# Kernel optimization log

Hardware: AMD Instinct MI355X
Metric: run time of the kernel (lower is better)

## Reference

```python
import jax, jax.numpy as jnp
import numpy as np

H = 8      # heads
D = 64     # dim_head
N0 = 1024  # modality-0 tokens
N1 = 1024  # modality-1 tokens
N = N0 + N1  # == token_num
DI = H * D   # dim_inner = 512


def setup_inputs() -> dict:
    key = jax.random.key(0)
    ks = jax.random.split(key, 10)
    s = 0.02
    return {
        "x0": jax.random.normal(ks[0], (1, N0, 512), jnp.float32),
        "x1": jax.random.normal(ks[1], (1, N1, 512), jnp.float32),
        "mask0": jnp.ones((1, N0), jnp.bool_),
        "mask1": jnp.ones((1, N1), jnp.bool_),
        "attn_dist": jax.random.normal(ks[2], (1, N, N), jnp.float32),
        "W_in0": jax.random.normal(ks[3], (512, 3 * DI), jnp.float32) * s,
        "W_in1": jax.random.normal(ks[4], (512, 3 * DI), jnp.float32) * s,
        "W_tau": jax.random.normal(ks[5], (DI, N * H), jnp.float32) * s,
        "b_tau": jax.random.normal(ks[6], (N * H,), jnp.float32) * s,
        "W_out0": jax.random.normal(ks[7], (DI, 512), jnp.float32) * s,
        "W_out1": jax.random.normal(ks[8], (DI, 512), jnp.float32) * s,
    }


def _split_heads(qkv, B, n):
    # (B, n, 3*H*D) -> (3, B, H, n, D)   [matches Rearrange 'b n (qkv h d) -> qkv b h n d']
    return qkv.reshape(B, n, 3, H, D).transpose(2, 0, 3, 1, 4)


def reference(x0, x1, mask0, mask1, attn_dist, W_in0, W_in1, W_tau, b_tau, W_out0, W_out1):
    B = x0.shape[0]
    qkv0 = _split_heads(x0 @ W_in0, B, N0)
    qkv1 = _split_heads(x1 @ W_in1, B, N1)
    qkv = jnp.concatenate([qkv0, qkv1], axis=3)  # pack along token axis -> (3,B,H,N,D)
    q, k, v = qkv[0], qkv[1], qkv[2]
    mask = jnp.concatenate([mask0, mask1], axis=1)  # (B, N)

    sim = jnp.einsum('bhid,bhjd->bhij', q, k) / jnp.sqrt(jnp.array(D, q.dtype))
    neg = -jnp.finfo(sim.dtype).max
    sim = jnp.where(mask[:, None, None, :], sim, neg)

    # taus: raw row-major reshape of q (B,H,N,D) -> (B,N,H*D), as in torch .reshape
    q_flat = q.reshape(B, N, H * D)
    taus = (q_flat @ W_tau + b_tau).reshape(B, N, N, H)
    bias = (taus * attn_dist[..., None]).transpose(0, 3, 1, 2)  # (B,H,N,N)
    sim = sim - bias

    attn = jax.nn.softmax(sim.astype(jnp.float32), axis=-1).astype(sim.dtype)
    out = jnp.einsum('bhij,bhjd->bhid', attn, v)
    out = out.transpose(0, 2, 1, 3).reshape(B, N, H * D)  # merge heads

    out0 = out[:, :N0] @ W_out0
    out1 = out[:, N0:] @ W_out1
    return (out0, out1)
```

## Files before the change

kernel.cpp:

```cpp
#include <hip/hip_runtime.h>
#include <stdint.h>

typedef __bf16 bf16;
typedef __bf16 bf16x8 __attribute__((ext_vector_type(8)));
typedef float f32x4 __attribute__((ext_vector_type(4)));
typedef unsigned short u16x8 __attribute__((ext_vector_type(8)));

#define MFMA16(a, b, c) __builtin_amdgcn_mfma_f32_16x16x32_bf16(a, b, c, 0, 0, 0)

#define WAIT_VM8 0x0F78
#define WAIT_VM0 0x0F70

static __device__ __forceinline__ bf16x8 lds_frag(const unsigned short* p) {
  return __builtin_bit_cast(bf16x8, *(const u16x8*)p);
}

static __device__ __forceinline__ bf16x8 gmem_frag(const bf16* p) {
  return __builtin_bit_cast(bf16x8, *(const u16x8*)p);
}

static __device__ __forceinline__ u16x8 cvt8(const float* p) {
  f32x4 a = *(const f32x4*)p;
  f32x4 b = *(const f32x4*)(p + 4);
  u16x8 r;
#pragma unroll
  for (int e = 0; e < 4; ++e) {
    r[e] = __builtin_bit_cast(unsigned short, (bf16)a[e]);
    r[4 + e] = __builtin_bit_cast(unsigned short, (bf16)b[e]);
  }
  return r;
}

__global__ __launch_bounds__(256) void prep_kernel(
    const float* __restrict__ Wti, const float* __restrict__ btau,
    const float* __restrict__ x0, const float* __restrict__ x1,
    const float* __restrict__ Win0, const float* __restrict__ Win1,
    const float* __restrict__ Wo0, const float* __restrict__ Wo1,
    bf16* __restrict__ Wto, float* __restrict__ bto, bf16* __restrict__ xb,
    bf16* __restrict__ Winb0, bf16* __restrict__ Winb1,
    bf16* __restrict__ Wob0, bf16* __restrict__ Wob1) {
  const int b = blockIdx.x;
  const int tid = threadIdx.x;
  __shared__ unsigned short shm[8 * 32 * 72];

  if (b < 512) {
    const int c0 = (b & 7) * 64;
    const int j0 = (b >> 3) * 32;
#pragma unroll
    for (int it = 0; it < 8; ++it) {
      int idx = it * 256 + tid;
      int c = idx >> 5, j = idx & 31;
      u16x8 v = cvt8(Wti + (size_t)(c0 + c) * 16384 + (j0 + j) * 8);
#pragma unroll
      for (int h = 0; h < 8; ++h) shm[(h * 32 + j) * 72 + c] = v[h];
    }
    __syncthreads();
#pragma unroll
    for (int it = 0; it < 8; ++it) {
      int chunk = it * 256 + tid;
      int row = chunk >> 3, ck = chunk & 7;
      int h = row >> 5, j = row & 31;
      u16x8 v = *(const u16x8*)&shm[row * 72 + ck * 8];
      *(u16x8*)((unsigned short*)Wto + (size_t)(h * 2048 + j0 + j) * 512 + c0 + ck * 8) = v;
    }
    if ((b & 7) == 0) {
      int j = tid >> 3, h = tid & 7;
      bto[h * 2048 + j0 + j] = btau[(j0 + j) * 8 + h];
    }
  } else if (b < 896) {
    int t = b - 512;
    const float* W = t < 192 ? Win0 : Win1;
    bf16* Wb = t < 192 ? Winb0 : Winb1;
    t = t < 192 ? t : t - 192;
    const int c0 = (t & 7) * 64, n0 = (t >> 3) * 64;
#pragma unroll
    for (int it = 0; it < 2; ++it) {
      int idx = it * 256 + tid;
      int c = idx >> 3, nn = idx & 7;
      u16x8 v = cvt8(W + (size_t)(c0 + c) * 1536 + n0 + nn * 8);
#pragma unroll
      for (int e = 0; e < 8; ++e) shm[(nn * 8 + e) * 72 + c] = v[e];
    }
    __syncthreads();
#pragma unroll
    for (int it = 0; it < 2; ++it) {
      int idx = it * 256 + tid;
      int n = idx >> 3, ck = idx & 7;
      *(u16x8*)((unsigned short*)Wb + (size_t)(n0 + n) * 512 + c0 + ck * 8) =
          *(const u16x8*)&shm[n * 72 + ck * 8];
    }
  } else if (b < 1408) {
    int t = b - 896;
    const float* src = t < 256 ? x0 : x1;
    size_t dst0 = t < 256 ? 0 : 524288;
    int tt = t < 256 ? t : t - 256;
    size_t off = (size_t)tt * 2048 + tid * 8;
    u16x8 v = cvt8(src + off);
    *(u16x8*)((unsigned short*)xb + dst0 + off) = v;
  } else {
    int t = b - 1408;
    const float* W = t < 64 ? Wo0 : Wo1;
    bf16* Wb = t < 64 ? Wob0 : Wob1;
    t &= 63;
    const int c0 = (t & 7) * 64, n0 = (t >> 3) * 64;
#pragma unroll
    for (int it = 0; it < 2; ++it) {
      int idx = it * 256 + tid;
      int c = idx >> 3, nn = idx & 7;
      u16x8 v = cvt8(W + (size_t)(c0 + c) * 512 + n0 + nn * 8);
#pragma unroll
      for (int e = 0; e < 8; ++e) shm[(nn * 8 + e) * 72 + c] = v[e];
    }
    __syncthreads();
#pragma unroll
    for (int it = 0; it < 2; ++it) {
      int idx = it * 256 + tid;
      int n = idx >> 3, ck = idx & 7;
      *(u16x8*)((unsigned short*)Wb + (size_t)(n0 + n) * 512 + c0 + ck * 8) =
          *(const u16x8*)&shm[n * 72 + ck * 8];
    }
  }
}

__global__ __launch_bounds__(256) void qkv_gemm(
    const bf16* __restrict__ xb, const bf16* __restrict__ Winb0, const bf16* __restrict__ Winb1,
    bf16* __restrict__ Qb, bf16* __restrict__ Kb, bf16* __restrict__ Vt_g) {
  const int i0 = blockIdx.x * 128, c0 = blockIdx.y * 128;
  const bf16* Bm = (i0 < 1024) ? Winb0 : Winb1;
  const int tid = threadIdx.x;
  const int lane = tid & 63, wave = tid >> 6;
  const int l16 = lane & 15, quad = lane >> 4;
  const int mrow = (wave & 1) * 64, ncol = (wave >> 1) * 64;
  __shared__ unsigned short As[2][128 * 64];
  __shared__ unsigned short Bs[2][128 * 64];
  f32x4 acc[4][4] = {};

#define QKV_STAGE(bb, kt)                                                               \
  do {                                                                                  \
    const int k0s = (kt) * 64;                                                          \
    _Pragma("unroll") for (int c = 0; c < 4; ++c) {                                     \
      int s = c * 256 + tid;                                                            \
      int row = s >> 3, pos = s & 7;                                                    \
      int kc = pos ^ (row & 7);                                                         \
      __builtin_amdgcn_global_load_lds(                                                 \
          (const unsigned int*)(xb + (size_t)(i0 + row) * 512 + k0s + kc * 8),          \
          (unsigned int*)&As[bb][s * 8], 16, 0, 0);                                     \
      __builtin_amdgcn_global_load_lds(                                                 \
          (const unsigned int*)(Bm + (size_t)(c0 + row) * 512 + k0s + kc * 8),          \
          (unsigned int*)&Bs[bb][s * 8], 16, 0, 0);                                     \
    }                                                                                   \
  } while (0)

  QKV_STAGE(0, 0);
  for (int t = 0; t < 8; ++t) {
    const int cur = t & 1;
    if (t < 7) {
      QKV_STAGE(cur ^ 1, t + 1);
      __builtin_amdgcn_s_waitcnt(WAIT_VM8);
    } else {
      __builtin_amdgcn_s_waitcnt(WAIT_VM0);
    }
    __builtin_amdgcn_s_barrier();
#pragma unroll
    for (int kb = 0; kb < 2; ++kb) {
      bf16x8 a[4], b[4];
#pragma unroll
      for (int mt = 0; mt < 4; ++mt) {
        int row = mrow + mt * 16 + l16;
        a[mt] = lds_frag(&As[cur][row * 64 + (((kb * 4 + quad) ^ (row & 7)) * 8)]);
      }
#pragma unroll
      for (int nt = 0; nt < 4; ++nt) {
        int row = ncol + nt * 16 + l16;
        b[nt] = lds_frag(&Bs[cur][row * 64 + (((kb * 4 + quad) ^ (row & 7)) * 8)]);
      }
#pragma unroll
      for (int mt = 0; mt < 4; ++mt)
#pragma unroll
        for (int nt = 0; nt < 4; ++nt) acc[mt][nt] = MFMA16(a[mt], b[nt], acc[mt][nt]);
    }
    __builtin_amdgcn_s_barrier();
  }
  __builtin_amdgcn_sched_barrier(0);
#undef QKV_STAGE

#pragma unroll
  for (int mt = 0; mt < 4; ++mt)
#pragma unroll
    for (int nt = 0; nt < 4; ++nt)
#pragma unroll
      for (int r = 0; r < 4; ++r) {
        int row = i0 + mrow + mt * 16 + quad * 4 + r;
        int col = c0 + ncol + nt * 16 + l16;
        int qsel = col >> 9, h = (col >> 6) & 7, d = col & 63;
        bf16 val = (bf16)acc[mt][nt][r];
        if (qsel == 2) {
          Vt_g[(size_t)(h * 64 + d) * 2048 + row] = val;
        } else {
          bf16* dst = qsel == 0 ? Qb : Kb;
          dst[(size_t)(h * 2048 + row) * 64 + d] = val;
        }
      }
}

__global__ __launch_bounds__(256) void tau_gemm(
    const bf16* __restrict__ Qb, const bf16* __restrict__ Wt,
    const float* __restrict__ bt, const float* __restrict__ ad, bf16* __restrict__ T) {
  const int i0 = blockIdx.x * 128;
  const int j0 = blockIdx.y * 16;
  const int tid = threadIdx.x;
  const int lane = tid & 63, wave = tid >> 6;
  const int l16 = lane & 15, quad = lane >> 4;
  const int mrow = (wave & 1) * 64, ncol = (wave >> 1) * 64;
  __shared__ unsigned short As[2][128 * 64];
  __shared__ unsigned short Bs[2][128 * 64];
  f32x4 acc[4][4] = {};

#define TAU_STAGE(bb, kt)                                                                    \
  do {                                                                                       \
    const int k0s = (kt) * 64;                                                               \
    _Pragma("unroll") for (int c = 0; c < 4; ++c) {                                          \
      int s = c * 256 + tid;                                                                 \
      int row = s >> 3, pos = s & 7;                                                         \
      int kc = pos ^ (row & 7);                                                              \
      __builtin_amdgcn_global_load_lds(                                                      \
          (const unsigned int*)(Qb + (size_t)(i0 + row) * 512 + k0s + kc * 8),               \
          (unsigned int*)&As[bb][s * 8], 16, 0, 0);                                          \
      __builtin_amdgcn_global_load_lds(                                                      \
          (const unsigned int*)(Wt + (size_t)((row >> 4) * 2048 + j0 + (row & 15)) * 512 +   \
                                k0s + kc * 8),                                               \
          (unsigned int*)&Bs[bb][s * 8], 16, 0, 0);                                          \
    }                                                                                        \
  } while (0)

  TAU_STAGE(0, 0);
  for (int t = 0; t < 8; ++t) {
    const int cur = t & 1;
    if (t < 7) {
      TAU_STAGE(cur ^ 1, t + 1);
      __builtin_amdgcn_s_waitcnt(WAIT_VM8);
    } else {
      __builtin_amdgcn_s_waitcnt(WAIT_VM0);
    }
    __builtin_amdgcn_s_barrier();
#pragma unroll
    for (int kb = 0; kb < 2; ++kb) {
      bf16x8 a[4], b[4];
#pragma unroll
      for (int mt = 0; mt < 4; ++mt) {
        int row = mrow + mt * 16 + l16;
        a[mt] = lds_frag(&As[cur][row * 64 + (((kb * 4 + quad) ^ (row & 7)) * 8)]);
      }
#pragma unroll
      for (int nt = 0; nt < 4; ++nt) {
        int row = ncol + nt * 16 + l16;
        b[nt] = lds_frag(&Bs[cur][row * 64 + (((kb * 4 + quad) ^ (row & 7)) * 8)]);
      }
#pragma unroll
      for (int mt = 0; mt < 4; ++mt)
#pragma unroll
        for (int nt = 0; nt < 4; ++nt) acc[mt][nt] = MFMA16(a[mt], b[nt], acc[mt][nt]);
    }
    __builtin_amdgcn_s_barrier();
  }
  __builtin_amdgcn_sched_barrier(0);
#undef TAU_STAGE

  float btv[4];
  int hh[4];
#pragma unroll
  for (int nt = 0; nt < 4; ++nt) {
    int c = ncol + nt * 16 + l16;
    hh[nt] = c >> 4;
    btv[nt] = bt[hh[nt] * 2048 + j0 + l16];
  }
#pragma unroll
  for (int mt = 0; mt < 4; ++mt)
#pragma unroll
    for (int r = 0; r < 4; ++r) {
      int row = i0 + mrow + mt * 16 + quad * 4 + r;
      float av = ad[(size_t)row * 2048 + j0 + l16];
#pragma unroll
      for (int nt = 0; nt < 4; ++nt)
        T[(size_t)hh[nt] * 4194304 + (size_t)row * 2048 + j0 + l16] =
            (bf16)((acc[mt][nt][r] + btv[nt]) * av);
    }
}

__global__ __launch_bounds__(256) void attn_kernel(
    const bf16* __restrict__ Qb, const bf16* __restrict__ Kb, const bf16* __restrict__ Vt_g,
    const bf16* __restrict__ T, float* __restrict__ Op, float* __restrict__ Ml) {
  const int h = blockIdx.y;
  const int i0 = blockIdx.x * 64;
  const int js = blockIdx.z;
  const int tid = threadIdx.x;
  const int lane = tid & 63, wave = tid >> 6;
  const int l16 = lane & 15, quad = lane >> 4;
  __shared__ unsigned short Ks[64 * 64];
  __shared__ unsigned short Vt[64 * 64];
  __shared__ unsigned short Tb[64 * 64];
  __shared__ unsigned short Ps[64 * 72];

  const bf16* Kh = Kb + (size_t)h * (2048 * 64);
  const bf16* Vh = Vt_g + (size_t)h * (64 * 2048);
  const bf16* Th = T + (size_t)h * (2048 * 2048);

  bf16x8 aQ[2];
#pragma unroll
  for (int kk = 0; kk < 2; ++kk)
    aQ[kk] = gmem_frag(Qb + (size_t)(h * 2048 + i0 + wave * 16 + l16) * 64 + kk * 32 + quad * 8);
  f32x4 Oacc[4] = {};
  float m_run[4], l_run[4];
#pragma unroll
  for (int r = 0; r < 4; ++r) { m_run[r] = -3.0e38f; l_run[r] = 0.f; }
  const int rowl = wave * 16 + quad * 4;

  for (int t = 0; t < 8; ++t) {
    const int j0 = js * 512 + t * 64;
    __syncthreads();
#pragma unroll
    for (int c = 0; c < 2; ++c) {
      int s = c * 256 + tid;
      int r8 = s >> 3, pos = s & 7;
      int sc = pos ^ (r8 & 7);
      __builtin_amdgcn_global_load_lds(
          (const unsigned int*)(Kh + (size_t)(j0 + r8) * 64 + sc * 8),
          (unsigned int*)&Ks[s * 8], 16, 0, 0);
      __builtin_amdgcn_global_load_lds(
          (const unsigned int*)(Vh + (size_t)r8 * 2048 + j0 + sc * 8),
          (unsigned int*)&Vt[s * 8], 16, 0, 0);
      __builtin_amdgcn_global_load_lds(
          (const unsigned int*)(Th + (size_t)(i0 + r8) * 2048 + j0 + pos * 8),
          (unsigned int*)&Tb[s * 8], 16, 0, 0);
    }
    __syncthreads();

    f32x4 S[4] = {};
#pragma unroll
    for (int nt = 0; nt < 4; ++nt) {
      int row = nt * 16 + l16;
#pragma unroll
      for (int kk = 0; kk < 2; ++kk) {
        bf16x8 bk = lds_frag(&Ks[row * 64 + (((kk * 4 + quad) ^ (row & 7)) * 8)]);
        S[nt] = MFMA16(aQ[kk], bk, S[nt]);
      }
    }
    float sv[4][4];
#pragma unroll
    for (int nt = 0; nt < 4; ++nt)
#pragma unroll
      for (int r = 0; r < 4; ++r) {
        float tb = (float)__builtin_bit_cast(bf16, Tb[(rowl + r) * 64 + nt * 16 + l16]);
        sv[nt][r] = S[nt][r] * 0.125f - tb;
      }
#pragma unroll
    for (int r = 0; r < 4; ++r) {
      float mx = fmaxf(fmaxf(sv[0][r], sv[1][r]), fmaxf(sv[2][r], sv[3][r]));
#pragma unroll
      for (int o = 1; o < 16; o <<= 1) mx = fmaxf(mx, __shfl_xor(mx, o, 16));
      float mnew = fmaxf(m_run[r], mx);
      float alpha = __expf(m_run[r] - mnew);
      m_run[r] = mnew;
      float rs = 0.f;
#pragma unroll
      for (int nt = 0; nt < 4; ++nt) { sv[nt][r] = __expf(sv[nt][r] - mnew); rs += sv[nt][r]; }
#pragma unroll
      for (int o = 1; o < 16; o <<= 1) rs += __shfl_xor(rs, o, 16);
      l_run[r] = l_run[r] * alpha + rs;
#pragma unroll
      for (int dt = 0; dt < 4; ++dt) Oacc[dt][r] *= alpha;
    }
#pragma unroll
    for (int nt = 0; nt < 4; ++nt)
#pragma unroll
      for (int r = 0; r < 4; ++r)
        Ps[(rowl + r) * 72 + nt * 16 + l16] =
            __builtin_bit_cast(unsigned short, (bf16)sv[nt][r]);
    __builtin_amdgcn_s_waitcnt(0xC07F);
    __builtin_amdgcn_wave_barrier();
#pragma unroll
    for (int kk = 0; kk < 2; ++kk) {
      bf16x8 aP = lds_frag(&Ps[(wave * 16 + l16) * 72 + kk * 32 + quad * 8]);
#pragma unroll
      for (int dt = 0; dt < 4; ++dt) {
        int row = dt * 16 + l16;
        bf16x8 bv = lds_frag(&Vt[row * 64 + (((kk * 4 + quad) ^ (row & 7)) * 8)]);
        Oacc[dt] = MFMA16(aP, bv, Oacc[dt]);
      }
    }
    __builtin_amdgcn_wave_barrier();
  }
  const size_t pb = ((size_t)js * 8 + h) * 2048;
#pragma unroll
  for (int r = 0; r < 4; ++r) {
    int rowg = i0 + rowl + r;
#pragma unroll
    for (int dt = 0; dt < 4; ++dt)
      Op[(pb + rowg) * 64 + dt * 16 + l16] = Oacc[dt][r];
    if (l16 == 0) {
      Ml[(pb + rowg) * 2 + 0] = m_run[r];
      Ml[(pb + rowg) * 2 + 1] = l_run[r];
    }
  }
}

__global__ __launch_bounds__(256) void merge_kernel(
    const float* __restrict__ Op, const float* __restrict__ Ml, bf16* __restrict__ om) {
  const int gr = blockIdx.x * 4 + (threadIdx.x >> 6);
  const int d = threadIdx.x & 63;
  float ms[4];
  float mmax = -3.0e38f;
#pragma unroll
  for (int s = 0; s < 4; ++s) {
    ms[s] = Ml[((size_t)s * 16384 + gr) * 2 + 0];
    mmax = fmaxf(mmax, ms[s]);
  }
  float lsum = 0.f, o = 0.f;
#pragma unroll
  for (int s = 0; s < 4; ++s) {
    float w = __expf(ms[s] - mmax);
    lsum += Ml[((size_t)s * 16384 + gr) * 2 + 1] * w;
    o += Op[((size_t)s * 16384 + gr) * 64 + d] * w;
  }
  int h = gr >> 11, i = gr & 2047;
  om[(size_t)i * 512 + h * 64 + d] = (bf16)(o / lsum);
}

__global__ __launch_bounds__(256) void out_proj(
    const bf16* __restrict__ om, const bf16* __restrict__ Wob0, const bf16* __restrict__ Wob1,
    float* __restrict__ out) {
  const int mod = blockIdx.z;
  const bf16* Bw = mod ? Wob1 : Wob0;
  float* outp = out + (size_t)mod * (1024 * 512);
  const int i0 = blockIdx.x * 64, c0 = blockIdx.y * 64;
  const int grow0 = mod * 1024 + i0;
  const int tid = threadIdx.x;
  const int lane = tid & 63, wave = tid >> 6;
  const int l16 = lane & 15, quad = lane >> 4;
  const int mrow = (wave & 1) * 32, ncol = (wave >> 1) * 32;
  __shared__ unsigned short As[64 * 64];
  __shared__ unsigned short Bs[64 * 64];
  f32x4 acc[2][2] = {};

  for (int k0 = 0; k0 < 512; k0 += 64) {
    __syncthreads();
#pragma unroll
    for (int c = 0; c < 2; ++c) {
      int s = c * 256 + tid;
      int row = s >> 3, pos = s & 7;
      int kc = pos ^ (row & 7);
      __builtin_amdgcn_global_load_lds((const unsigned int*)(om + (size_t)(grow0 + row) * 512 + k0 + kc * 8),
                                       (unsigned int*)&As[s * 8], 16, 0, 0);
      __builtin_amdgcn_global_load_lds((const unsigned int*)(Bw + (size_t)(c0 + row) * 512 + k0 + kc * 8),
                                       (unsigned int*)&Bs[s * 8], 16, 0, 0);
    }
    __syncthreads();
#pragma unroll
    for (int kb = 0; kb < 2; ++kb) {
      bf16x8 a[2], b[2];
#pragma unroll
      for (int mt = 0; mt < 2; ++mt) {
        int row = mrow + mt * 16 + l16;
        a[mt] = lds_frag(&As[row * 64 + (((kb * 4 + quad) ^ (row & 7)) * 8)]);
      }
#pragma unroll
      for (int nt = 0; nt < 2; ++nt) {
        int row = ncol + nt * 16 + l16;
        b[nt] = lds_frag(&Bs[row * 64 + (((kb * 4 + quad) ^ (row & 7)) * 8)]);
      }
#pragma unroll
      for (int mt = 0; mt < 2; ++mt)
#pragma unroll
        for (int nt = 0; nt < 2; ++nt) acc[mt][nt] = MFMA16(a[mt], b[nt], acc[mt][nt]);
    }
  }
#pragma unroll
  for (int mt = 0; mt < 2; ++mt)
#pragma unroll
    for (int nt = 0; nt < 2; ++nt)
#pragma unroll
      for (int r = 0; r < 4; ++r) {
        int row = i0 + mrow + mt * 16 + quad * 4 + r;
        int col = c0 + ncol + nt * 16 + l16;
        outp[(size_t)row * 512 + col] = acc[mt][nt][r];
      }
}

extern "C" void kernel_launch(void* const* d_in, const int* in_sizes, int n_in,
                              void* d_out, int out_size, void* d_ws, size_t ws_size,
                              hipStream_t stream) {
  (void)in_sizes; (void)n_in; (void)out_size; (void)ws_size;
  const float* x0   = (const float*)d_in[0];
  const float* x1   = (const float*)d_in[1];
  const float* ad   = (const float*)d_in[4];
  const float* Win0 = (const float*)d_in[5];
  const float* Win1 = (const float*)d_in[6];
  const float* Wtau = (const float*)d_in[7];
  const float* btau = (const float*)d_in[8];
  const float* Wo0  = (const float*)d_in[9];
  const float* Wo1  = (const float*)d_in[10];
  float* out = (float*)d_out;

  bf16* ws = (bf16*)d_ws;
  bf16* Qb = ws;
  bf16* Kb = Qb + 1048576;
  bf16* Vt_g = Kb + 1048576;
  bf16* Wt = Vt_g + 1048576;
  bf16* T  = Wt + 8388608;
  bf16* om = T + 33554432;
  float* bt = (float*)(om + 1048576);
  float* Ml = bt + 16384;
  bf16* Wob0 = (bf16*)(Ml + 131072);
  bf16* Wob1 = Wob0 + 262144;
  float* Op = (float*)Wt;
  bf16* xb    = T;
  bf16* Winb0 = T + 1048576;
  bf16* Winb1 = Winb0 + 786432;

  prep_kernel<<<1536, 256, 0, stream>>>(Wtau, btau, x0, x1, Win0, Win1, Wo0, Wo1,
                                        Wt, bt, xb, Winb0, Winb1, Wob0, Wob1);
  qkv_gemm<<<dim3(16, 12), 256, 0, stream>>>(xb, Winb0, Winb1, Qb, Kb, Vt_g);
  tau_gemm<<<dim3(16, 128), 256, 0, stream>>>(Qb, Wt, bt, ad, T);
  attn_kernel<<<dim3(32, 8, 4), 256, 0, stream>>>(Qb, Kb, Vt_g, T, Op, Ml);
  merge_kernel<<<4096, 256, 0, stream>>>(Op, Ml, om);
  out_proj<<<dim3(16, 8, 2), 256, 0, stream>>>(om, Wob0, Wob1, out);
}
```

Before: 228.3 us.

## Double-buffer LDS tiles in attention and output projection kernels

Converts the K/V/T tiles in the attention kernel and the A/B tiles in the output projection to two LDS buffers. The next tile is prefetched with global_load_lds, and partial vmcnt waits let that load overlap compute on the current tile. This hides global memory latency behind MFMA work. In exchange it doubles LDS use, which may cut occupancy, and correctness depends on the hand-set vmcnt counts matching the number of outstanding loads.

```diff
diff --git a/kernel.cpp b/kernel.cpp
--- a/kernel.cpp
+++ b/kernel.cpp
@@ -9,6 +9,8 @@
 #define MFMA16(a, b, c) __builtin_amdgcn_mfma_f32_16x16x32_bf16(a, b, c, 0, 0, 0)
 
 #define WAIT_VM8 0x0F78
+#define WAIT_VM6 0x0F76
+#define WAIT_VM4 0x0F74
 #define WAIT_VM0 0x0F70
 
 static __device__ __forceinline__ bf16x8 lds_frag(const unsigned short* p) {
@@ -296,14 +298,33 @@
   const int tid = threadIdx.x;
   const int lane = tid & 63, wave = tid >> 6;
   const int l16 = lane & 15, quad = lane >> 4;
-  __shared__ unsigned short Ks[64 * 64];
-  __shared__ unsigned short Vt[64 * 64];
-  __shared__ unsigned short Tb[64 * 64];
+  __shared__ unsigned short Ks[2][64 * 64];
+  __shared__ unsigned short Vt[2][64 * 64];
+  __shared__ unsigned short Tb[2][64 * 64];
   __shared__ unsigned short Ps[64 * 72];
 
   const bf16* Kh = Kb + (size_t)h * (2048 * 64);
   const bf16* Vh = Vt_g + (size_t)h * (64 * 2048);
   const bf16* Th = T + (size_t)h * (2048 * 2048);
+
+#define ATTN_STAGE(bb, tt)                                                        \
+  do {                                                                            \
+    const int j0s = js * 512 + (tt) * 64;                                         \
+    _Pragma("unroll") for (int c = 0; c < 2; ++c) {                               \
+      int s = c * 256 + tid;                                                      \
+      int r8 = s >> 3, pos = s & 7;                                               \
+      int sc = pos ^ (r8 & 7);                                                    \
+      __builtin_amdgcn_global_load_lds(                                           \
+          (const unsigned int*)(Kh + (size_t)(j0s + r8) * 64 + sc * 8),           \
+          (unsigned int*)&Ks[bb][s * 8], 16, 0, 0);                               \
+      __builtin_amdgcn_global_load_lds(                                           \
+          (const unsigned int*)(Vh + (size_t)r8 * 2048 + j0s + sc * 8),           \
+          (unsigned int*)&Vt[bb][s * 8], 16, 0, 0);                               \
+      __builtin_amdgcn_global_load_lds(                                           \
+          (const unsigned int*)(Th + (size_t)(i0 + r8) * 2048 + j0s + pos * 8),   \
+          (unsigned int*)&Tb[bb][s * 8], 16, 0, 0);                               \
+    }                                                                             \
+  } while (0)
 
   bf16x8 aQ[2];
 #pragma unroll
@@ -315,25 +336,16 @@
   for (int r = 0; r < 4; ++r) { m_run[r] = -3.0e38f; l_run[r] = 0.f; }
   const int rowl = wave * 16 + quad * 4;
 
+  ATTN_STAGE(0, 0);
   for (int t = 0; t < 8; ++t) {
-    const int j0 = js * 512 + t * 64;
-    __syncthreads();
-#pragma unroll
-    for (int c = 0; c < 2; ++c) {
-      int s = c * 256 + tid;
-      int r8 = s >> 3, pos = s & 7;
-      int sc = pos ^ (r8 & 7);
-      __builtin_amdgcn_global_load_lds(
-          (const unsigned int*)(Kh + (size_t)(j0 + r8) * 64 + sc * 8),
-          (unsigned int*)&Ks[s * 8], 16, 0, 0);
-      __builtin_amdgcn_global_load_lds(
-          (const unsigned int*)(Vh + (size_t)r8 * 2048 + j0 + sc * 8),
-          (unsigned int*)&Vt[s * 8], 16, 0, 0);
-      __builtin_amdgcn_global_load_lds(
-          (const unsigned int*)(Th + (size_t)(i0 + r8) * 2048 + j0 + pos * 8),
-          (unsigned int*)&Tb[s * 8], 16, 0, 0);
-    }
-    __syncthreads();
+    const int cur = t & 1;
+    if (t < 7) {
+      ATTN_STAGE(cur ^ 1, t + 1);
+      __builtin_amdgcn_s_waitcnt(WAIT_VM6);
+    } else {
+      __builtin_amdgcn_s_waitcnt(WAIT_VM0);
+    }
+    __builtin_amdgcn_s_barrier();
 
     f32x4 S[4] = {};
 #pragma unroll
@@ -341,7 +353,7 @@
       int row = nt * 16 + l16;
 #pragma unroll
       for (int kk = 0; kk < 2; ++kk) {
-        bf16x8 bk = lds_frag(&Ks[row * 64 + (((kk * 4 + quad) ^ (row & 7)) * 8)]);
+        bf16x8 bk = lds_frag(&Ks[cur][row * 64 + (((kk * 4 + quad) ^ (row & 7)) * 8)]);
         S[nt] = MFMA16(aQ[kk], bk, S[nt]);
       }
     }
@@ -350,7 +362,7 @@
     for (int nt = 0; nt < 4; ++nt)
 #pragma unroll
       for (int r = 0; r < 4; ++r) {
-        float tb = (float)__builtin_bit_cast(bf16, Tb[(rowl + r) * 64 + nt * 16 + l16]);
+        float tb = (float)__builtin_bit_cast(bf16, Tb[cur][(rowl + r) * 64 + nt * 16 + l16]);
         sv[nt][r] = S[nt][r] * 0.125f - tb;
       }
 #pragma unroll
@@ -384,12 +396,14 @@
 #pragma unroll
       for (int dt = 0; dt < 4; ++dt) {
         int row = dt * 16 + l16;
-        bf16x8 bv = lds_frag(&Vt[row * 64 + (((kk * 4 + quad) ^ (row & 7)) * 8)]);
+        bf16x8 bv = lds_frag(&Vt[cur][row * 64 + (((kk * 4 + quad) ^ (row & 7)) * 8)]);
         Oacc[dt] = MFMA16(aP, bv, Oacc[dt]);
       }
     }
     __builtin_amdgcn_wave_barrier();
-  }
+    __builtin_amdgcn_s_barrier();
+  }
+#undef ATTN_STAGE
   const size_t pb = ((size_t)js * 8 + h) * 2048;
 #pragma unroll
   for (int r = 0; r < 4; ++r) {
@@ -438,42 +452,59 @@
   const int lane = tid & 63, wave = tid >> 6;
   const int l16 = lane & 15, quad = lane >> 4;
   const int mrow = (wave & 1) * 32, ncol = (wave >> 1) * 32;
-  __shared__ unsigned short As[64 * 64];
-  __shared__ unsigned short Bs[64 * 64];
+  __shared__ unsigned short As[2][64 * 64];
+  __shared__ unsigned short Bs[2][64 * 64];
   f32x4 acc[2][2] = {};
 
-  for (int k0 = 0; k0 < 512; k0 += 64) {
-    __syncthreads();
-#pragma unroll
-    for (int c = 0; c < 2; ++c) {
-      int s = c * 256 + tid;
-      int row = s >> 3, pos = s & 7;
-      int kc = pos ^ (row & 7);
-      __builtin_amdgcn_global_load_lds((const unsigned int*)(om + (size_t)(grow0 + row) * 512 + k0 + kc * 8),
-                                       (unsigned int*)&As[s * 8], 16, 0, 0);
-      __builtin_amdgcn_global_load_lds((const unsigned int*)(Bw + (size_t)(c0 + row) * 512 + k0 + kc * 8),
-                                       (unsigned int*)&Bs[s * 8], 16, 0, 0);
-    }
-    __syncthreads();
+#define OUT_STAGE(bb, kt)                                                               \
+  do {                                                                                  \
+    const int k0s = (kt) * 64;                                                          \
+    _Pragma("unroll") for (int c = 0; c < 2; ++c) {                                     \
+      int s = c * 256 + tid;                                                            \
+      int row = s >> 3, pos = s & 7;                                                    \
+      int kc = pos ^ (row & 7);                                                         \
+      __builtin_amdgcn_global_load_lds(                                                 \
+          (const unsigned int*)(om + (size_t)(grow0 + row) * 512 + k0s + kc * 8),       \
+          (unsigned int*)&As[bb][s * 8], 16, 0, 0);                                     \
+      __builtin_amdgcn_global_load_lds(                                                 \
+          (const unsigned int*)(Bw + (size_t)(c0 + row) * 512 + k0s + kc * 8),          \
+          (unsigned int*)&Bs[bb][s * 8], 16, 0, 0);                                     \
+    }                                                                                   \
+  } while (0)
+
+  OUT_STAGE(0, 0);
+  for (int t = 0; t < 8; ++t) {
+    const int cur = t & 1;
+    if (t < 7) {
+      OUT_STAGE(cur ^ 1, t + 1);
+      __builtin_amdgcn_s_waitcnt(WAIT_VM4);
+    } else {
+      __builtin_amdgcn_s_waitcnt(WAIT_VM0);
+    }
+    __builtin_amdgcn_s_barrier();
 #pragma unroll
     for (int kb = 0; kb < 2; ++kb) {
       bf16x8 a[2], b[2];
 #pragma unroll
       for (int mt = 0; mt < 2; ++mt) {
         int row = mrow + mt * 16 + l16;
-        a[mt] = lds_frag(&As[row * 64 + (((kb * 4 + quad) ^ (row & 7)) * 8)]);
+        a[mt] = lds_frag(&As[cur][row * 64 + (((kb * 4 + quad) ^ (row & 7)) * 8)]);
       }
 #pragma unroll
       for (int nt = 0; nt < 2; ++nt) {
         int row = ncol + nt * 16 + l16;
-        b[nt] = lds_frag(&Bs[row * 64 + (((kb * 4 + quad) ^ (row & 7)) * 8)]);
+        b[nt] = lds_frag(&Bs[cur][row * 64 + (((kb * 4 + quad) ^ (row & 7)) * 8)]);
       }
 #pragma unroll
       for (int mt = 0; mt < 2; ++mt)
 #pragma unroll
         for (int nt = 0; nt < 2; ++nt) acc[mt][nt] = MFMA16(a[mt], b[nt], acc[mt][nt]);
     }
-  }
+    __builtin_amdgcn_s_barrier();
+  }
+  __builtin_amdgcn_sched_barrier(0);
+#undef OUT_STAGE
+
 #pragma unroll
   for (int mt = 0; mt < 2; ++mt)
 #pragma unroll
```

Result: slower. 236.0 us (+3.3%).

## Store bias tensor in MFMA-fragment tiled layout and load directly to registers

Applied to the files above, without the earlier changes.

The tau-bias producer now writes T in a per-(head, 64x64 tile) layout where each attention thread's 16 needed elements are contiguous, packing four bf16 values per store. The attention kernel then reads its bias fragment with two 16-byte global loads straight into registers, instead of staging the 64x64 tile through LDS and reading it element by element. This removes one LDS buffer, the staging loads and the scattered LDS reads. In exchange, producer stores become 8-byte writes with a different access pattern, and the bias loads are now synchronous register loads issued in the loop.

```diff
diff --git a/kernel.cpp b/kernel.cpp
--- a/kernel.cpp
+++ b/kernel.cpp
@@ -5,6 +5,7 @@
 typedef __bf16 bf16x8 __attribute__((ext_vector_type(8)));
 typedef float f32x4 __attribute__((ext_vector_type(4)));
 typedef unsigned short u16x8 __attribute__((ext_vector_type(8)));
+typedef unsigned short u16x4 __attribute__((ext_vector_type(4)));
 
 #define MFMA16(a, b, c) __builtin_amdgcn_mfma_f32_16x16x32_bf16(a, b, c, 0, 0, 0)
 
@@ -274,17 +275,26 @@
     hh[nt] = c >> 4;
     btv[nt] = bt[hh[nt] * 2048 + j0 + l16];
   }
-#pragma unroll
-  for (int mt = 0; mt < 4; ++mt)
-#pragma unroll
-    for (int r = 0; r < 4; ++r) {
-      int row = i0 + mrow + mt * 16 + quad * 4 + r;
-      float av = ad[(size_t)row * 2048 + j0 + l16];
-#pragma unroll
-      for (int nt = 0; nt < 4; ++nt)
-        T[(size_t)hh[nt] * 4194304 + (size_t)row * 2048 + j0 + l16] =
-            (bf16)((acc[mt][nt][r] + btv[nt]) * av);
-    }
+  const int Ibase = (i0 + mrow) >> 6;
+  const int J = j0 >> 6;
+  const int eoff = ((j0 >> 4) & 3) * 4;
+  const int atq = quad * 16 + l16;
+#pragma unroll
+  for (int mt = 0; mt < 4; ++mt) {
+    float av[4];
+#pragma unroll
+    for (int r = 0; r < 4; ++r)
+      av[r] = ad[(size_t)(i0 + mrow + mt * 16 + quad * 4 + r) * 2048 + j0 + l16];
+#pragma unroll
+    for (int nt = 0; nt < 4; ++nt) {
+      u16x4 pk;
+#pragma unroll
+      for (int r = 0; r < 4; ++r)
+        pk[r] = __builtin_bit_cast(unsigned short, (bf16)((acc[mt][nt][r] + btv[nt]) * av[r]));
+      size_t tile = (size_t)hh[nt] * 1024 + Ibase * 32 + J;
+      *(u16x4*)((unsigned short*)T + tile * 4096 + (mt * 64 + atq) * 16 + eoff) = pk;
+    }
+  }
 }
 
 __global__ __launch_bounds__(256) void attn_kernel(
@@ -298,12 +308,12 @@
   const int l16 = lane & 15, quad = lane >> 4;
   __shared__ unsigned short Ks[64 * 64];
   __shared__ unsigned short Vt[64 * 64];
-  __shared__ unsigned short Tb[64 * 64];
   __shared__ unsigned short Ps[64 * 72];
 
   const bf16* Kh = Kb + (size_t)h * (2048 * 64);
   const bf16* Vh = Vt_g + (size_t)h * (64 * 2048);
-  const bf16* Th = T + (size_t)h * (2048 * 2048);
+  const unsigned short* Tp = (const unsigned short*)T +
+      (((size_t)h * 1024 + (size_t)(i0 >> 6) * 32) * 4096) + (size_t)tid * 16;
 
   bf16x8 aQ[2];
 #pragma unroll
@@ -318,6 +328,9 @@
   for (int t = 0; t < 8; ++t) {
     const int j0 = js * 512 + t * 64;
     __syncthreads();
+    const unsigned short* tp = Tp + (size_t)(js * 8 + t) * 4096;
+    u16x8 tb01 = *(const u16x8*)tp;
+    u16x8 tb23 = *(const u16x8*)(tp + 8);
 #pragma unroll
     for (int c = 0; c < 2; ++c) {
       int s = c * 256 + tid;
@@ -329,9 +342,6 @@
       __builtin_amdgcn_global_load_lds(
           (const unsigned int*)(Vh + (size_t)r8 * 2048 + j0 + sc * 8),
           (unsigned int*)&Vt[s * 8], 16, 0, 0);
-      __builtin_amdgcn_global_load_lds(
-          (const unsigned int*)(Th + (size_t)(i0 + r8) * 2048 + j0 + pos * 8),
-          (unsigned int*)&Tb[s * 8], 16, 0, 0);
     }
     __syncthreads();
 
@@ -350,7 +360,9 @@
     for (int nt = 0; nt < 4; ++nt)
 #pragma unroll
       for (int r = 0; r < 4; ++r) {
-        float tb = (float)__builtin_bit_cast(bf16, Tb[(rowl + r) * 64 + nt * 16 + l16]);
+        int e = nt * 4 + r;
+        unsigned short tbu = e < 8 ? tb01[e] : tb23[e - 8];
+        float tb = (float)__builtin_bit_cast(bf16, tbu);
         sv[nt][r] = S[nt][r] * 0.125f - tb;
       }
 #pragma unroll
```

Result: no change. 225.8 us (-1.1%).
